# Kernel optimization log

Hardware: AMD Instinct MI355X
Metric: run time of the kernel (lower is better)

The kernel has to match this reference:

```python
import jax, jax.numpy as jnp
import numpy as np
import jax.lax as lax
from jax.scipy.special import logsumexp

N, T, C = 512, 1024, 64  # batch, seq len, n_classes


def setup_inputs() -> dict:
    key = jax.random.key(0)
    k1, k2, k3, k4 = jax.random.split(key, 4)
    batch_logits = jax.random.normal(k1, (N, T, C), dtype=jnp.float32)
    # learned CRF transition matrix; (i,j) = score of transitioning j -> i
    transition_matrix = jax.random.normal(k2, (C, C), dtype=jnp.float32) * 0.1
    init_alphas = jnp.zeros((C,), dtype=jnp.float32)
    lengths = jax.random.randint(k3, (N,), 2, T + 1)
    batch_tags = jax.random.randint(k4, (N, T), 0, C)
    return dict(batch_logits=batch_logits, transition_matrix=transition_matrix,
                init_alphas=init_alphas, lengths=lengths, batch_tags=batch_tags)


def _log_partition_scores(trans, init_alphas, logits):
    """sum_scores: logZ of all sequences of length (i+2), shape [T-1]."""
    def step(prev_alphas, logit_t):
        # core_recursion with fn=logsumexp: [C,1] + [C,C] + [1,C] -> lse over axis 1
        new = logsumexp(logit_t[:, None] + trans + prev_alphas[None, :], axis=1)
        return new, logsumexp(new, axis=-1)
    _, scores = lax.scan(step, init_alphas + logits[0], logits[1:])
    return scores


def _gold_scores(trans, init_alphas, logits, tags):
    """score_sequence: score of gold prefix of length (i+2), shape [T-1]."""
    first = init_alphas[tags[0]] + logits[0, tags[0]]
    # step increments: transition[tags[t+1], tags[t]] + logits[t+1, tags[t+1]]
    steps = trans[tags[1:], tags[:-1]] + \
        jnp.take_along_axis(logits[1:], tags[1:, None], axis=1)[:, 0]
    return first + jnp.cumsum(steps)


def reference(batch_logits, transition_matrix, init_alphas, lengths, batch_tags):
    # CRF negative log-likelihood per sequence: logZ(length) - gold_score(length)
    logZ_all = jax.vmap(lambda lg: _log_partition_scores(transition_matrix, init_alphas, lg))(batch_logits)
    gold_all = jax.vmap(lambda lg, tg: _gold_scores(transition_matrix, init_alphas, lg, tg))(batch_logits, batch_tags)
    idx = (lengths - 2)[:, None]  # pick the entry at the true sequence length
    logZ = jnp.take_along_axis(logZ_all, idx, axis=1)[:, 0]
    gold = jnp.take_along_axis(gold_all, idx, axis=1)[:, 0]
    return logZ - gold  # [N]
```

## Files before the change

### kernel.cpp

```cpp
#include <hip/hip_runtime.h>
#include <cstdint>
#include <cstddef>

#define NC 64
#define LN2 0.6931471805599453f

typedef _Float16 half2_t __attribute__((ext_vector_type(2)));
typedef unsigned int uint32x4 __attribute__((ext_vector_type(4)));

static __device__ __forceinline__ float dot2acc(uint32_t a, uint32_t b, float c) {
#if __has_builtin(__builtin_amdgcn_fdot2)
    return __builtin_amdgcn_fdot2(__builtin_bit_cast(half2_t, a),
                                  __builtin_bit_cast(half2_t, b), c, false);
#else
    half2_t ha = __builtin_bit_cast(half2_t, a), hb = __builtin_bit_cast(half2_t, b);
    return c + (float)ha[0] * (float)hb[0] + (float)ha[1] * (float)hb[1];
#endif
}

template <int CTRL>
static __device__ __forceinline__ uint32_t dpp_mov(uint32_t x) {
    return (uint32_t)__builtin_amdgcn_update_dpp(0, (int)x, CTRL, 0xf, 0xf, true);
}
template <int CTRL>
static __device__ __forceinline__ float dppf(float x) {
    return __int_as_float(__builtin_amdgcn_update_dpp(
        0, __float_as_int(x), CTRL, 0xf, 0xf, true));
}
static __device__ __forceinline__ float wave_sum_bcast(float x) {
    x = x + dppf<0x111>(x);
    x = x + dppf<0x112>(x);
    x = x + dppf<0x114>(x);
    x = x + dppf<0x118>(x);
    x = x + dppf<0x142>(x);
    x = x + dppf<0x143>(x);
    return __int_as_float(__builtin_amdgcn_readlane(__float_as_int(x), 63));
}


__global__ __launch_bounds__(128, 1)
void crf_nll_kernel(const float* __restrict__ logits,
                    const float* __restrict__ trans,
                    const float* __restrict__ init_alphas,
                    const int*  __restrict__ lengths,
                    const int*  __restrict__ tags,
                    float* __restrict__ out,
                    int N, int T)
{
    const int n = blockIdx.x;
    const int tid = threadIdx.x;
    const int wid = tid >> 6;
    const int lane = tid & 63;
    const float* lg = logits + (size_t)n * T * NC;
    const int len = lengths[n];
    const int Tm1 = T - 1;

    __shared__ __align__(16) uint32_t Etab[2][64 * 32];
    __shared__ __align__(16) float xchg[2][NC];
    __shared__ float Lsh[2], gsh[2];

    #pragma unroll
    for (int idx = tid; idx < 2 * 64 * 32; idx += 128) {
        int tab = idx >> 11, rem = idx & 2047;
        int i = rem >> 5, wrd = rem & 31;
        int j = wrd >> 2, k = wrd & 3;
        int D = (j & 3) | ((j & 4) << 1);
        int row = i ^ D;
        int s = (i & 3) | ((i >> 1) & 4);
        int c0 = 8 * s + 2 * k, c1 = c0 + 1;
        float x0 = tab == 0 ? trans[row * NC + c0] : trans[c0 * NC + row];
        float x1 = tab == 0 ? trans[row * NC + c1] : trans[c1 * NC + row];
        uint32_t lo = (uint32_t)__builtin_bit_cast(uint16_t, (_Float16)__expf(x0));
        uint32_t hi = (uint32_t)__builtin_bit_cast(uint16_t, (_Float16)__expf(x1));
        Etab[tab][i * 32 + wrd] = lo | (hi << 16);
    }
    __syncthreads();

    uint32x4 e0, e1, e2, e3, e4, e5, e6, e7;
    {
        uint32_t e_addr = (uint32_t)(uintptr_t)&Etab[wid][0] + (uint32_t)(lane * 128);
        asm volatile(
            "ds_read_b128 %0, %8 offset:0\n\t"
            "ds_read_b128 %1, %8 offset:16\n\t"
            "ds_read_b128 %2, %8 offset:32\n\t"
            "ds_read_b128 %3, %8 offset:48\n\t"
            "ds_read_b128 %4, %8 offset:64\n\t"
            "ds_read_b128 %5, %8 offset:80\n\t"
            "ds_read_b128 %6, %8 offset:96\n\t"
            "ds_read_b128 %7, %8 offset:112\n\t"
            "s_waitcnt lgkmcnt(0)"
            : "=&v"(e0), "=&v"(e1), "=&v"(e2), "=&v"(e3),
              "=&v"(e4), "=&v"(e5), "=&v"(e6), "=&v"(e7)
            : "v"(e_addr)
            : "memory");
        __builtin_amdgcn_sched_barrier(0);
    }

    const int m  = (len - 1) >> 1;
    const int nb = len - 1 - m;

    const int s_lane = (lane & 3) | ((lane >> 1) & 4);
    const int ba0 = 32 * s_lane;
    const int ba1 = ba0 + 8;
    const int ba2 = ba0 + 16;
    const int ba3 = ba0 + 24;

    float L = 0.f, vcur = 1.0f, s_cur = 1.0f, dL = 0.0f;

    auto dotE = [&](float vv) -> float {
        uint32_t c16 = (uint32_t)__builtin_bit_cast(uint16_t, (_Float16)vv);
        uint32_t nbr = dpp_mov<0xB1>(c16);
        uint32_t h = c16 | (nbr << 16);
        uint32_t wx = (uint32_t)__builtin_amdgcn_ds_bpermute(ba0, (int)h);
        uint32_t wy = (uint32_t)__builtin_amdgcn_ds_bpermute(ba1, (int)h);
        uint32_t wz = (uint32_t)__builtin_amdgcn_ds_bpermute(ba2, (int)h);
        uint32_t ww = (uint32_t)__builtin_amdgcn_ds_bpermute(ba3, (int)h);
        float p0, p1, p2, p3, p4, p5, p6, p7;
        p0 = dot2acc(e0.x, wx, dot2acc(e0.y, wy, dot2acc(e0.z, wz, dot2acc(e0.w, ww, 0.f))));
        p1 = dot2acc(e1.x, wx, dot2acc(e1.y, wy, dot2acc(e1.z, wz, dot2acc(e1.w, ww, 0.f))));
        p2 = dot2acc(e2.x, wx, dot2acc(e2.y, wy, dot2acc(e2.z, wz, dot2acc(e2.w, ww, 0.f))));
        p3 = dot2acc(e3.x, wx, dot2acc(e3.y, wy, dot2acc(e3.z, wz, dot2acc(e3.w, ww, 0.f))));
        p4 = dot2acc(e4.x, wx, dot2acc(e4.y, wy, dot2acc(e4.z, wz, dot2acc(e4.w, ww, 0.f))));
        p5 = dot2acc(e5.x, wx, dot2acc(e5.y, wy, dot2acc(e5.z, wz, dot2acc(e5.w, ww, 0.f))));
        p6 = dot2acc(e6.x, wx, dot2acc(e6.y, wy, dot2acc(e6.z, wz, dot2acc(e6.w, ww, 0.f))));
        p7 = dot2acc(e7.x, wx, dot2acc(e7.y, wy, dot2acc(e7.z, wz, dot2acc(e7.w, ww, 0.f))));
        float q0  = p0 + dppf<0xB1>(p1);
        float q2  = p2 + dppf<0xB1>(p3);
        float q8  = p4 + dppf<0xB1>(p5);
        float q10 = p6 + dppf<0xB1>(p7);
        float r0 = q0 + dppf<0x4E>(q2);
        float r8 = q8 + dppf<0x4E>(q10);
        float t8 = dppf<0x141>(r8);
        return r0 + dppf<0x140>(t8);
    };

    if (wid == 0) {
        float a0 = init_alphas[lane] + lg[lane];
        L = __int_as_float(__builtin_amdgcn_readfirstlane(__float_as_int(a0))) + 8.f * LN2;
        vcur = __expf(a0 - L);

        auto fstep = [&](float raw) {
            float fs = __expf(raw) * s_cur;
            L += dL;
            float v = fs * dotE(vcur);
            vcur = v;
            unsigned bits = (unsigned)__builtin_amdgcn_readfirstlane((int)__float_as_uint(v));
            int e = (int)((bits >> 23) & 0xFF);
            s_cur = __uint_as_float((unsigned)(246 - e) << 23);
            dL    = (float)(e - 119) * LN2;
        };

        float r0 = lg[NC * (1 < Tm1 ? 1 : Tm1) + lane];
        float r1 = lg[NC * (2 < Tm1 ? 2 : Tm1) + lane];
        float r2 = lg[NC * (3 < Tm1 ? 3 : Tm1) + lane];
        float r3 = lg[NC * (4 < Tm1 ? 4 : Tm1) + lane];
        float r4 = lg[NC * (5 < Tm1 ? 5 : Tm1) + lane];
        float r5 = lg[NC * (6 < Tm1 ? 6 : Tm1) + lane];
        float r6 = lg[NC * (7 < Tm1 ? 7 : Tm1) + lane];
        float r7 = lg[NC * (8 < Tm1 ? 8 : Tm1) + lane];

        int t = 1;
        for (; t + 8 <= m + 1; t += 8) {
            int p;
            fstep(r0); p = t +  8; p = p < Tm1 ? p : Tm1; r0 = lg[NC * p + lane];
            fstep(r1); p = t +  9; p = p < Tm1 ? p : Tm1; r1 = lg[NC * p + lane];
            fstep(r2); p = t + 10; p = p < Tm1 ? p : Tm1; r2 = lg[NC * p + lane];
            fstep(r3); p = t + 11; p = p < Tm1 ? p : Tm1; r3 = lg[NC * p + lane];
            fstep(r4); p = t + 12; p = p < Tm1 ? p : Tm1; r4 = lg[NC * p + lane];
            fstep(r5); p = t + 13; p = p < Tm1 ? p : Tm1; r5 = lg[NC * p + lane];
            fstep(r6); p = t + 14; p = p < Tm1 ? p : Tm1; r6 = lg[NC * p + lane];
            fstep(r7); p = t + 15; p = p < Tm1 ? p : Tm1; r7 = lg[NC * p + lane];
        }
        if (t + 0 <= m) fstep(r0);
        if (t + 1 <= m) fstep(r1);
        if (t + 2 <= m) fstep(r2);
        if (t + 3 <= m) fstep(r3);
        if (t + 4 <= m) fstep(r4);
        if (t + 5 <= m) fstep(r5);
        if (t + 6 <= m) fstep(r6);
    } else {
        auto bstep = [&](float raw) {
            float p = __expf(raw) * s_cur * vcur;
            L += dL;
            float u = dotE(p);
            vcur = u;
            unsigned bits = (unsigned)__builtin_amdgcn_readfirstlane((int)__float_as_uint(u));
            int e = (int)((bits >> 23) & 0xFF);
            s_cur = __uint_as_float((unsigned)(246 - e) << 23);
            dL    = (float)(e - 119) * LN2;
        };

        int p0i;
        p0i = len - 1; p0i = p0i > 1 ? p0i : 1; float r0 = lg[NC * p0i + lane];
        p0i = len - 2; p0i = p0i > 1 ? p0i : 1; float r1 = lg[NC * p0i + lane];
        p0i = len - 3; p0i = p0i > 1 ? p0i : 1; float r2 = lg[NC * p0i + lane];
        p0i = len - 4; p0i = p0i > 1 ? p0i : 1; float r3 = lg[NC * p0i + lane];
        p0i = len - 5; p0i = p0i > 1 ? p0i : 1; float r4 = lg[NC * p0i + lane];
        p0i = len - 6; p0i = p0i > 1 ? p0i : 1; float r5 = lg[NC * p0i + lane];
        p0i = len - 7; p0i = p0i > 1 ? p0i : 1; float r6 = lg[NC * p0i + lane];
        p0i = len - 8; p0i = p0i > 1 ? p0i : 1; float r7 = lg[NC * p0i + lane];

        int k = 0;
        for (; k + 8 <= nb; k += 8) {
            int p;
            bstep(r0); p = len - 1 - (k +  8); p = p > 1 ? p : 1; r0 = lg[NC * p + lane];
            bstep(r1); p = len - 1 - (k +  9); p = p > 1 ? p : 1; r1 = lg[NC * p + lane];
            bstep(r2); p = len - 1 - (k + 10); p = p > 1 ? p : 1; r2 = lg[NC * p + lane];
            bstep(r3); p = len - 1 - (k + 11); p = p > 1 ? p : 1; r3 = lg[NC * p + lane];
            bstep(r4); p = len - 1 - (k + 12); p = p > 1 ? p : 1; r4 = lg[NC * p + lane];
            bstep(r5); p = len - 1 - (k + 13); p = p > 1 ? p : 1; r5 = lg[NC * p + lane];
            bstep(r6); p = len - 1 - (k + 14); p = p > 1 ? p : 1; r6 = lg[NC * p + lane];
            bstep(r7); p = len - 1 - (k + 15); p = p > 1 ? p : 1; r7 = lg[NC * p + lane];
        }
        if (k + 0 < nb) bstep(r0);
        if (k + 1 < nb) bstep(r1);
        if (k + 2 < nb) bstep(r2);
        if (k + 3 < nb) bstep(r3);
        if (k + 4 < nb) bstep(r4);
        if (k + 5 < nb) bstep(r5);
        if (k + 6 < nb) bstep(r6);
    }

    xchg[wid][lane] = vcur;
    if (lane == 0) Lsh[wid] = L;

    const int* tg = tags + (size_t)n * T;
    float g = 0.f;
    for (int tt = 1 + tid; tt < len; tt += 128) {
        const int cur = tg[tt];
        const int prv = tg[tt - 1];
        g += trans[cur * NC + prv] + lg[tt * NC + cur];
    }
    g = wave_sum_bcast(g);
    if (lane == 0) gsh[wid] = g;

    __syncthreads();

    if (wid == 0) {
        float prod = xchg[0][lane] * xchg[1][lane];
        float ssum = wave_sum_bcast(prod);
        if (lane == 0) {
            float logZ = Lsh[0] + Lsh[1] + __logf(ssum);
            int t0v = tg[0];
            float gold = init_alphas[t0v] + lg[t0v] + gsh[0] + gsh[1];
            out[n] = logZ - gold;
        }
    }
}

extern "C" void kernel_launch(void* const* d_in, const int* in_sizes, int n_in,
                              void* d_out, int out_size, void* d_ws, size_t ws_size,
                              hipStream_t stream)
{
    const float* logits = (const float*)d_in[0];
    const float* trans  = (const float*)d_in[1];
    const float* inita  = (const float*)d_in[2];
    const int*   lens   = (const int*)d_in[3];
    const int*   tags   = (const int*)d_in[4];
    float*       out    = (float*)d_out;

    const int N = 512, T = 1024;
    crf_nll_kernel<<<N, 128, 0, stream>>>(logits, trans, inita, lens, tags, out, N, T);
}
```

Before: 149.9 us.

## Replace ds_bpermute broadcast with permlane swap exchange and matching table layout

Result: slower. 160.7 us (+7.2%).

```diff
diff --git a/kernel.cpp b/kernel.cpp
--- a/kernel.cpp
+++ b/kernel.cpp
@@ -35,6 +35,31 @@
     x = x + dppf<0x142>(x);
     x = x + dppf<0x143>(x);
     return __int_as_float(__builtin_amdgcn_readlane(__float_as_int(x), 63));
+}
+
+static __device__ __forceinline__ void pl32_pair(uint32_t src, uint32_t& o0, uint32_t& o1) {
+    uint32_t a, b;
+    asm("v_mov_b32 %0, %2\n\t"
+        "v_mov_b32 %1, %2\n\t"
+        "v_permlane32_swap_b32 %0, %1"
+        : "=&v"(a), "=&v"(b) : "v"(src));
+    o0 = a; o1 = b;
+}
+static __device__ __forceinline__ void pl16_pair(uint32_t src, uint32_t& o0, uint32_t& o1) {
+    uint32_t a, b;
+    asm("v_mov_b32 %0, %2\n\t"
+        "v_mov_b32 %1, %2\n\t"
+        "v_permlane16_swap_b32 %0, %1"
+        : "=&v"(a), "=&v"(b) : "v"(src));
+    o0 = a; o1 = b;
+}
+
+static __device__ __forceinline__ void exchange(uint32_t h, uint32_t& b0, uint32_t& b1,
+                                                uint32_t& b2, uint32_t& b3) {
+    uint32_t a, b;
+    pl32_pair(h, a, b);
+    pl16_pair(a, b0, b1);
+    pl16_pair(b, b2, b3);
 }
 
 
@@ -59,20 +84,29 @@
     __shared__ __align__(16) float xchg[2][NC];
     __shared__ float Lsh[2], gsh[2];
 
-    #pragma unroll
-    for (int idx = tid; idx < 2 * 64 * 32; idx += 128) {
-        int tab = idx >> 11, rem = idx & 2047;
-        int i = rem >> 5, wrd = rem & 31;
-        int j = wrd >> 2, k = wrd & 3;
-        int D = (j & 3) | ((j & 4) << 1);
-        int row = i ^ D;
-        int s = (i & 3) | ((i >> 1) & 4);
-        int c0 = 8 * s + 2 * k, c1 = c0 + 1;
-        float x0 = tab == 0 ? trans[row * NC + c0] : trans[c0 * NC + row];
-        float x1 = tab == 0 ? trans[row * NC + c1] : trans[c1 * NC + row];
-        uint32_t lo = (uint32_t)__builtin_bit_cast(uint16_t, (_Float16)__expf(x0));
-        uint32_t hi = (uint32_t)__builtin_bit_cast(uint16_t, (_Float16)__expf(x1));
-        Etab[tab][i * 32 + wrd] = lo | (hi << 16);
+    uint32_t pb0, pb1, pb2, pb3;
+    {
+        uint32_t hp = (uint32_t)lane | (((uint32_t)(lane ^ 1)) << 16);
+        exchange(hp, pb0, pb1, pb2, pb3);
+    }
+
+    {
+        uint32_t pq[4] = {pb0, pb1, pb2, pb3};
+        uint32_t* dst = &Etab[wid][lane * 32];
+        #pragma unroll
+        for (int d = 0; d < 8; ++d) {
+            int row = lane ^ (2 * d);
+            #pragma unroll
+            for (int q = 0; q < 4; ++q) {
+                int j_lo = (int)(pq[q] & 0xFFFFu);
+                int j_hi = (int)(pq[q] >> 16);
+                float xlo = wid == 0 ? trans[row * NC + j_lo] : trans[j_lo * NC + row];
+                float xhi = wid == 0 ? trans[row * NC + j_hi] : trans[j_hi * NC + row];
+                uint32_t lo = (uint32_t)__builtin_bit_cast(uint16_t, (_Float16)__expf(xlo));
+                uint32_t hi = (uint32_t)__builtin_bit_cast(uint16_t, (_Float16)__expf(xhi));
+                dst[d * 4 + q] = lo | (hi << 16);
+            }
+        }
     }
     __syncthreads();
 
@@ -99,39 +133,29 @@
     const int m  = (len - 1) >> 1;
     const int nb = len - 1 - m;
 
-    const int s_lane = (lane & 3) | ((lane >> 1) & 4);
-    const int ba0 = 32 * s_lane;
-    const int ba1 = ba0 + 8;
-    const int ba2 = ba0 + 16;
-    const int ba3 = ba0 + 24;
-
     float L = 0.f, vcur = 1.0f, s_cur = 1.0f, dL = 0.0f;
 
     auto dotE = [&](float vv) -> float {
         uint32_t c16 = (uint32_t)__builtin_bit_cast(uint16_t, (_Float16)vv);
-        uint32_t nbr = dpp_mov<0xB1>(c16);
-        uint32_t h = c16 | (nbr << 16);
-        uint32_t wx = (uint32_t)__builtin_amdgcn_ds_bpermute(ba0, (int)h);
-        uint32_t wy = (uint32_t)__builtin_amdgcn_ds_bpermute(ba1, (int)h);
-        uint32_t wz = (uint32_t)__builtin_amdgcn_ds_bpermute(ba2, (int)h);
-        uint32_t ww = (uint32_t)__builtin_amdgcn_ds_bpermute(ba3, (int)h);
+        uint32_t h = c16 | (dpp_mov<0xB1>(c16) << 16);
+        uint32_t b0, b1, b2, b3;
+        exchange(h, b0, b1, b2, b3);
         float p0, p1, p2, p3, p4, p5, p6, p7;
-        p0 = dot2acc(e0.x, wx, dot2acc(e0.y, wy, dot2acc(e0.z, wz, dot2acc(e0.w, ww, 0.f))));
-        p1 = dot2acc(e1.x, wx, dot2acc(e1.y, wy, dot2acc(e1.z, wz, dot2acc(e1.w, ww, 0.f))));
-        p2 = dot2acc(e2.x, wx, dot2acc(e2.y, wy, dot2acc(e2.z, wz, dot2acc(e2.w, ww, 0.f))));
-        p3 = dot2acc(e3.x, wx, dot2acc(e3.y, wy, dot2acc(e3.z, wz, dot2acc(e3.w, ww, 0.f))));
-        p4 = dot2acc(e4.x, wx, dot2acc(e4.y, wy, dot2acc(e4.z, wz, dot2acc(e4.w, ww, 0.f))));
-        p5 = dot2acc(e5.x, wx, dot2acc(e5.y, wy, dot2acc(e5.z, wz, dot2acc(e5.w, ww, 0.f))));
-        p6 = dot2acc(e6.x, wx, dot2acc(e6.y, wy, dot2acc(e6.z, wz, dot2acc(e6.w, ww, 0.f))));
-        p7 = dot2acc(e7.x, wx, dot2acc(e7.y, wy, dot2acc(e7.z, wz, dot2acc(e7.w, ww, 0.f))));
-        float q0  = p0 + dppf<0xB1>(p1);
-        float q2  = p2 + dppf<0xB1>(p3);
-        float q8  = p4 + dppf<0xB1>(p5);
-        float q10 = p6 + dppf<0xB1>(p7);
-        float r0 = q0 + dppf<0x4E>(q2);
-        float r8 = q8 + dppf<0x4E>(q10);
-        float t8 = dppf<0x141>(r8);
-        return r0 + dppf<0x140>(t8);
+        p0 = dot2acc(e0.x, b0, dot2acc(e0.y, b1, dot2acc(e0.z, b2, dot2acc(e0.w, b3, 0.f))));
+        p1 = dot2acc(e1.x, b0, dot2acc(e1.y, b1, dot2acc(e1.z, b2, dot2acc(e1.w, b3, 0.f))));
+        p2 = dot2acc(e2.x, b0, dot2acc(e2.y, b1, dot2acc(e2.z, b2, dot2acc(e2.w, b3, 0.f))));
+        p3 = dot2acc(e3.x, b0, dot2acc(e3.y, b1, dot2acc(e3.z, b2, dot2acc(e3.w, b3, 0.f))));
+        p4 = dot2acc(e4.x, b0, dot2acc(e4.y, b1, dot2acc(e4.z, b2, dot2acc(e4.w, b3, 0.f))));
+        p5 = dot2acc(e5.x, b0, dot2acc(e5.y, b1, dot2acc(e5.z, b2, dot2acc(e5.w, b3, 0.f))));
+        p6 = dot2acc(e6.x, b0, dot2acc(e6.y, b1, dot2acc(e6.z, b2, dot2acc(e6.w, b3, 0.f))));
+        p7 = dot2acc(e7.x, b0, dot2acc(e7.y, b1, dot2acc(e7.z, b2, dot2acc(e7.w, b3, 0.f))));
+        float q0  = p0 + dppf<0x4E>(p1);
+        float q4  = p2 + dppf<0x4E>(p3);
+        float q8  = p4 + dppf<0x4E>(p5);
+        float q12 = p6 + dppf<0x4E>(p7);
+        float r0 = q0 + dppf<0x1B>(dppf<0x141>(q4));
+        float r8 = q8 + dppf<0x1B>(dppf<0x141>(q12));
+        return r0 + dppf<0x140>(dppf<0x141>(r8));
     };
 
     if (wid == 0) {
```
